# Kernel optimization log

Measured on AMD Instinct MI355X. Metric: run time of the kernel, lower is better.

Reference implementation:

```python
import jax, jax.numpy as jnp
import numpy as np

B, N, D = 32768, 256, 3


def setup_inputs() -> dict:
    key = jax.random.key(0)
    k1, k2 = jax.random.split(key)
    keypoints = jax.random.normal(k1, (B, N, D), dtype=jnp.float32)
    perm = jax.random.permutation(k2, B)  # emulates torch.randperm, deterministic
    return {"keypoints": keypoints, "perm": perm}


def _transform_a2b(src, dst):
    # src, dst: [B, N, 3]; batched similarity (Umeyama/Kabsch-style) alignment.
    num = src.shape[1]
    src_mean = src.mean(axis=1)                     # [B, 3]
    dst_mean = dst.mean(axis=1)                     # [B, 3]
    src_d = src - src_mean[:, None]                 # [B, N, 3]
    dst_d = dst - dst_mean[:, None]                 # [B, N, 3]
    A = jnp.einsum('bni,bnj->bij', dst_d, src_d) / num  # [B, 3, 3] covariance
    U, S, Vt = jnp.linalg.svd(A)
    # NOTE: in the original torch code `d[neg_A][:, -1, -1] = -1` writes into a
    # COPY (advanced indexing), so d stays identity for all batches. We
    # faithfully reproduce that actual behavior: R = U @ V^T, scale uses sum(S).
    var_sum = jnp.mean(jnp.sum(src_d * src_d, axis=-1), axis=1)  # sum of per-dim biased var
    scale = jnp.sum(S, axis=-1) / var_sum           # [B]
    R = U @ Vt                                      # [B, 3, 3]
    T = dst_mean - scale[:, None] * jnp.einsum('bij,bj->bi', R, src_mean)  # [B, 3]
    # Original computes R, scale, T under torch.no_grad().
    R = jax.lax.stop_gradient(R)
    scale = jax.lax.stop_gradient(scale)
    T = jax.lax.stop_gradient(T)
    return src @ (jnp.swapaxes(R, -1, -2) * scale[:, None, None]) + T[:, None]


def reference(keypoints, perm):
    dst = keypoints[perm]                            # randomized keypoints
    trans = _transform_a2b(keypoints, dst)
    return jnp.mean(jnp.abs(trans - dst))
```

## Files before the change

kernel.cpp:

```cpp
#include <hip/hip_runtime.h>
#include <math.h>

#define GEO_N 256

__device__ __forceinline__ float frcp(float x) { return __builtin_amdgcn_rcpf(x); }
__device__ __forceinline__ float frsq(float x) { return __builtin_amdgcn_rsqf(x); }
__device__ __forceinline__ float fsqrtf_(float x) { return __builtin_amdgcn_sqrtf(x); }

__device__ __forceinline__ float wredf(float v) {
#pragma unroll
  for (int off = 32; off; off >>= 1) v += __shfl_xor(v, off, 64);
  return v;
}

template <int P, int Q>
__device__ __forceinline__ void jrot(float G[3][3], float V[3][3]) {
  const float apq = G[P][Q];
  const float tau = (G[Q][Q] - G[P][P]) * 0.5f * frcp(apq);
  const float tt = fsqrtf_(1.0f + tau * tau);
  const float tr = frcp(tau + copysignf(tt, tau));
  const float cr = frsq(1.0f + tr * tr);
  const bool skip = fabsf(apq) < 1e-30f;
  const float c = skip ? 1.0f : cr;
  const float s = skip ? 0.0f : tr * cr;
#pragma unroll
  for (int k = 0; k < 3; ++k) {
    float gkp = G[k][P], gkq = G[k][Q];
    G[k][P] = c * gkp - s * gkq;
    G[k][Q] = s * gkp + c * gkq;
  }
#pragma unroll
  for (int k = 0; k < 3; ++k) {
    float gpk = G[P][k], gqk = G[Q][k];
    G[P][k] = c * gpk - s * gqk;
    G[Q][k] = s * gpk + c * gqk;
  }
#pragma unroll
  for (int k = 0; k < 3; ++k) {
    float vkp = V[k][P], vkq = V[k][Q];
    V[k][P] = c * vkp - s * vkq;
    V[k][Q] = s * vkp + c * vkq;
  }
}

__device__ __forceinline__ void solve_rst(const float s0[16], float bc[13]) {
  const float invN = 1.0f / (float)GEO_N;
  const float smx = s0[0] * invN, smy = s0[1] * invN, smz = s0[2] * invN;
  const float dmx = s0[3] * invN, dmy = s0[4] * invN, dmz = s0[5] * invN;
  float A[3][3];
  A[0][0] = s0[6] * invN - dmx * smx;  A[0][1] = s0[7] * invN - dmx * smy;  A[0][2] = s0[8] * invN - dmx * smz;
  A[1][0] = s0[9] * invN - dmy * smx;  A[1][1] = s0[10] * invN - dmy * smy; A[1][2] = s0[11] * invN - dmy * smz;
  A[2][0] = s0[12] * invN - dmz * smx; A[2][1] = s0[13] * invN - dmz * smy; A[2][2] = s0[14] * invN - dmz * smz;
  const float var_sum = s0[15] * invN - (smx * smx + smy * smy + smz * smz);

  float G[3][3];
#pragma unroll
  for (int i = 0; i < 3; ++i)
#pragma unroll
    for (int j = 0; j < 3; ++j)
      G[i][j] = A[0][i] * A[0][j] + A[1][i] * A[1][j] + A[2][i] * A[2][j];
  float V[3][3] = {{1, 0, 0}, {0, 1, 0}, {0, 0, 1}};
#pragma unroll
  for (int sweep = 0; sweep < 4; ++sweep) {
    jrot<0, 1>(G, V);
    jrot<0, 2>(G, V);
    jrot<1, 2>(G, V);
  }
  float l0 = G[0][0], l1 = G[1][1], l2 = G[2][2];
  if (l0 < l1) { float tl = l0; l0 = l1; l1 = tl;
#pragma unroll
    for (int k = 0; k < 3; ++k) { float tv = V[k][0]; V[k][0] = V[k][1]; V[k][1] = tv; } }
  if (l0 < l2) { float tl = l0; l0 = l2; l2 = tl;
#pragma unroll
    for (int k = 0; k < 3; ++k) { float tv = V[k][0]; V[k][0] = V[k][2]; V[k][2] = tv; } }
  if (l1 < l2) { float tl = l1; l1 = l2; l2 = tl;
#pragma unroll
    for (int k = 0; k < 3; ++k) { float tv = V[k][1]; V[k][1] = V[k][2]; V[k][2] = tv; } }
  const float sig0 = fsqrtf_(fmaxf(l0, 0.0f));
  const float sig1 = fsqrtf_(fmaxf(l1, 0.0f));
  const float sig2 = fsqrtf_(fmaxf(l2, 0.0f));

  float v0[3] = {V[0][0], V[1][0], V[2][0]};
  float v1[3] = {V[0][1], V[1][1], V[2][1]};
  float v2[3] = {V[0][2], V[1][2], V[2][2]};
  float u0[3], u1[3], u2r[3];
#pragma unroll
  for (int i = 0; i < 3; ++i) {
    u0[i]  = A[i][0] * v0[0] + A[i][1] * v0[1] + A[i][2] * v0[2];
    u1[i]  = A[i][0] * v1[0] + A[i][1] * v1[1] + A[i][2] * v1[2];
    u2r[i] = A[i][0] * v2[0] + A[i][1] * v2[1] + A[i][2] * v2[2];
  }
  float n0 = u0[0] * u0[0] + u0[1] * u0[1] + u0[2] * u0[2];
  if (n0 > 1e-28f) { float inv = frsq(n0); u0[0] *= inv; u0[1] *= inv; u0[2] *= inv; }
  else { u0[0] = 1.0f; u0[1] = 0.0f; u0[2] = 0.0f; }
  float d01 = u1[0] * u0[0] + u1[1] * u0[1] + u1[2] * u0[2];
  u1[0] -= d01 * u0[0]; u1[1] -= d01 * u0[1]; u1[2] -= d01 * u0[2];
  float n1 = u1[0] * u1[0] + u1[1] * u1[1] + u1[2] * u1[2];
  if (n1 > 1e-28f) { float inv = frsq(n1); u1[0] *= inv; u1[1] *= inv; u1[2] *= inv; }
  else {
    float ex[3] = {1, 0, 0}, ey[3] = {0, 1, 0};
    const float* e = (fabsf(u0[0]) < 0.9f) ? ex : ey;
    u1[0] = u0[1] * e[2] - u0[2] * e[1];
    u1[1] = u0[2] * e[0] - u0[0] * e[2];
    u1[2] = u0[0] * e[1] - u0[1] * e[0];
    float nn = u1[0] * u1[0] + u1[1] * u1[1] + u1[2] * u1[2];
    float inv = frsq(nn);
    u1[0] *= inv; u1[1] *= inv; u1[2] *= inv;
  }
  float u2[3] = {u0[1] * u1[2] - u0[2] * u1[1],
                 u0[2] * u1[0] - u0[0] * u1[2],
                 u0[0] * u1[1] - u0[1] * u1[0]};
  float d2 = u2[0] * u2r[0] + u2[1] * u2r[1] + u2[2] * u2r[2];
  if (d2 < 0.0f) { u2[0] = -u2[0]; u2[1] = -u2[1]; u2[2] = -u2[2]; }

  const float scale = (sig0 + sig1 + sig2) * frcp(fmaxf(var_sum, 1e-30f));
  float R[3][3];
#pragma unroll
  for (int i = 0; i < 3; ++i)
#pragma unroll
    for (int j = 0; j < 3; ++j)
      R[i][j] = u0[i] * v0[j] + u1[i] * v1[j] + u2[i] * v2[j];
  const float Tx = dmx - scale * (R[0][0] * smx + R[0][1] * smy + R[0][2] * smz);
  const float Ty = dmy - scale * (R[1][0] * smx + R[1][1] * smy + R[1][2] * smz);
  const float Tz = dmz - scale * (R[2][0] * smx + R[2][1] * smy + R[2][2] * smz);
#pragma unroll
  for (int i = 0; i < 3; ++i)
#pragma unroll
    for (int j = 0; j < 3; ++j) bc[3 * i + j] = R[i][j];
  bc[9] = scale; bc[10] = Tx; bc[11] = Ty; bc[12] = Tz;
}

__global__ __launch_bounds__(256) void geo_wave4p(const float* __restrict__ kp,
                                                  const int* __restrict__ perm,
                                                  float* __restrict__ partials,
                                                  int B, int NW) {
  const int wid = (blockIdx.x << 2) | (threadIdx.x >> 6);
  if (wid >= NW) return;
  const int lane = threadIdx.x & 63;
  const int b0 = wid * 4;
  const float4* base = (const float4*)kp;

  int pm[4];
#pragma unroll
  for (int i = 0; i < 4; ++i) pm[i] = perm[min(b0 + i, B - 1)];

  float4 S[4][3], D[4][3];
  float parked = 0.0f;

#define GEO_LOAD(i)                                                        \
  {                                                                        \
    const int bb = min(b0 + (i), B - 1);                                   \
    const float4* s4 = base + (size_t)bb * 192 + lane * 3;                 \
    const float4* d4 = base + (size_t)pm[(i)] * 192 + lane * 3;            \
    S[(i)][0] = s4[0]; S[(i)][1] = s4[1]; S[(i)][2] = s4[2];               \
    D[(i)][0] = d4[0]; D[(i)][1] = d4[1]; D[(i)][2] = d4[2];               \
  }

#define GEO_MOM(i)                                                         \
  {                                                                        \
    const float s_[12] = {S[(i)][0].x, S[(i)][0].y, S[(i)][0].z, S[(i)][0].w, \
                          S[(i)][1].x, S[(i)][1].y, S[(i)][1].z, S[(i)][1].w, \
                          S[(i)][2].x, S[(i)][2].y, S[(i)][2].z, S[(i)][2].w}; \
    const float d_[12] = {D[(i)][0].x, D[(i)][0].y, D[(i)][0].z, D[(i)][0].w, \
                          D[(i)][1].x, D[(i)][1].y, D[(i)][1].z, D[(i)][1].w, \
                          D[(i)][2].x, D[(i)][2].y, D[(i)][2].z, D[(i)][2].w}; \
    float r[16];                                                           \
    _Pragma("unroll") for (int k = 0; k < 16; ++k) r[k] = 0.0f;            \
    _Pragma("unroll") for (int p = 0; p < 4; ++p) {                        \
      const float sx = s_[3 * p + 0], sy = s_[3 * p + 1], sz = s_[3 * p + 2]; \
      const float dx = d_[3 * p + 0], dy = d_[3 * p + 1], dz = d_[3 * p + 2]; \
      r[0] += sx; r[1] += sy; r[2] += sz;                                  \
      r[3] += dx; r[4] += dy; r[5] += dz;                                  \
      r[6] += dx * sx; r[7] += dx * sy; r[8] += dx * sz;                   \
      r[9] += dy * sx; r[10] += dy * sy; r[11] += dy * sz;                 \
      r[12] += dz * sx; r[13] += dz * sy; r[14] += dz * sz;                \
      r[15] += sx * sx + sy * sy + sz * sz;                                \
    }                                                                      \
     \
    const int b1 = lane & 1, b2 = (lane >> 1) & 1, b3 = (lane >> 2) & 1, b4 = (lane >> 3) & 1; \
    float v8[8], v4_[4], v2[2], v1;                                        \
    _Pragma("unroll") for (int k = 0; k < 8; ++k) {                        \
      float send = b1 ? r[k] : r[k + 8];                                   \
      float recv = __shfl_xor(send, 1, 64);                                \
      v8[k] = (b1 ? r[k + 8] : r[k]) + recv;                               \
    }                                                                      \
    _Pragma("unroll") for (int k = 0; k < 4; ++k) {                        \
      float send = b2 ? v8[k] : v8[k + 4];                                 \
      float recv = __shfl_xor(send, 2, 64);                                \
      v4_[k] = (b2 ? v8[k + 4] : v8[k]) + recv;                            \
    }                                                                      \
    _Pragma("unroll") for (int k = 0; k < 2; ++k) {                        \
      float send = b3 ? v4_[k] : v4_[k + 2];                               \
      float recv = __shfl_xor(send, 4, 64);                                \
      v2[k] = (b3 ? v4_[k + 2] : v4_[k]) + recv;                           \
    }                                                                      \
    {                                                                      \
      float send = b4 ? v2[0] : v2[1];                                     \
      float recv = __shfl_xor(send, 8, 64);                                \
      v1 = (b4 ? v2[1] : v2[0]) + recv;                                    \
    }                                                                      \
    v1 += __shfl_xor(v1, 16, 64);                                          \
    v1 += __shfl_xor(v1, 32, 64);                                          \
    if ((lane >> 4) == (i)) parked = v1;                                   \
  }

  GEO_LOAD(0)
  GEO_LOAD(1)
  __builtin_amdgcn_sched_barrier(0);
  GEO_MOM(0)
  GEO_LOAD(2)
  __builtin_amdgcn_sched_barrier(0);
  GEO_MOM(1)
  GEO_LOAD(3)
  __builtin_amdgcn_sched_barrier(0);
  GEO_MOM(2)
  __builtin_amdgcn_sched_barrier(0);
  GEO_MOM(3)

#undef GEO_LOAD
#undef GEO_MOM

  constexpr int br[16] = {0, 8, 4, 12, 2, 10, 6, 14, 1, 9, 5, 13, 3, 11, 7, 15};
  float s0[16];
#pragma unroll
  for (int k = 0; k < 16; ++k)
    s0[k] = __shfl(parked, ((lane & 3) << 4) | br[k], 64);

  float bc[13];
  solve_rst(s0, bc);

  float acc = 0.0f;
#pragma unroll
  for (int i = 0; i < 4; ++i) {
    const float R00 = __shfl(bc[0], i, 64), R01 = __shfl(bc[1], i, 64), R02 = __shfl(bc[2], i, 64);
    const float R10 = __shfl(bc[3], i, 64), R11 = __shfl(bc[4], i, 64), R12 = __shfl(bc[5], i, 64);
    const float R20 = __shfl(bc[6], i, 64), R21 = __shfl(bc[7], i, 64), R22 = __shfl(bc[8], i, 64);
    const float sc  = __shfl(bc[9], i, 64);
    const float Tx  = __shfl(bc[10], i, 64), Ty = __shfl(bc[11], i, 64), Tz = __shfl(bc[12], i, 64);
    const float s[12] = {S[i][0].x, S[i][0].y, S[i][0].z, S[i][0].w,
                         S[i][1].x, S[i][1].y, S[i][1].z, S[i][1].w,
                         S[i][2].x, S[i][2].y, S[i][2].z, S[i][2].w};
    const float d[12] = {D[i][0].x, D[i][0].y, D[i][0].z, D[i][0].w,
                         D[i][1].x, D[i][1].y, D[i][1].z, D[i][1].w,
                         D[i][2].x, D[i][2].y, D[i][2].z, D[i][2].w};
    float a = 0.0f;
#pragma unroll
    for (int q = 0; q < 4; ++q) {
      const float sx = s[3 * q + 0], sy = s[3 * q + 1], sz = s[3 * q + 2];
      const float dx = d[3 * q + 0], dy = d[3 * q + 1], dz = d[3 * q + 2];
      const float e0 = sc * (R00 * sx + R01 * sy + R02 * sz) + Tx - dx;
      const float e1 = sc * (R10 * sx + R11 * sy + R12 * sz) + Ty - dy;
      const float e2 = sc * (R20 * sx + R21 * sy + R22 * sz) + Tz - dz;
      a += fabsf(e0) + fabsf(e1) + fabsf(e2);
    }
    if (b0 + i < B) acc += a;
  }
  acc = wredf(acc);
  if (lane == 0) partials[wid] = acc;
}

__global__ __launch_bounds__(1024) void geo_fin(const float* __restrict__ partials,
                                                float* __restrict__ out, int n,
                                                double inv_total) {
  const int t = threadIdx.x;
  double acc = 0.0;
  for (int i = t; i < n; i += 1024) acc += (double)partials[i];
#pragma unroll
  for (int off = 32; off; off >>= 1) acc += __shfl_xor(acc, off, 64);
  __shared__ double sred[16];
  if ((t & 63) == 0) sred[t >> 6] = acc;
  __syncthreads();
  if (t == 0) {
    double tot = 0.0;
#pragma unroll
    for (int k = 0; k < 16; ++k) tot += sred[k];
    out[0] = (float)(tot * inv_total);
  }
}

extern "C" void kernel_launch(void* const* d_in, const int* in_sizes, int n_in,
                              void* d_out, int out_size, void* d_ws, size_t ws_size,
                              hipStream_t stream) {
  const float* kp = (const float*)d_in[0];
  const int* perm = (const int*)d_in[1];
  float* out = (float*)d_out;
  const int B = in_sizes[1];
  const double inv_total = 1.0 / ((double)B * (double)GEO_N * 3.0);

  const int NW = (B + 3) / 4;
  float* partials = (float*)d_ws;
  const int grid = (NW + 3) / 4;
  geo_wave4p<<<grid, 256, 0, stream>>>(kp, perm, partials, B, NW);
  geo_fin<<<1, 1024, 0, stream>>>(partials, out, NW, inv_total);
}
```

Baseline: 43.44 us.

## Replace Jacobi SVD with closed-form eigen solve and polar rotation

Replaces the 4-sweep Jacobi eigen-decomposition of A^T A with the analytic trigonometric eigenvalue formula for symmetric 3x3 matrices. It uses polynomial approximations of acos and cos, gets two eigenvectors from cross products, and forms R = A (A^T A)^{-1/2} directly instead of building U. This removes many serial rcp/sqrt-heavy rotations per batch in the solve phase. In exchange it risks accuracy for near-degenerate or rank-deficient covariances, and the sign handling differs from the explicit U construction. The v2 rename only avoids a name clash in the macro.

```diff
diff --git a/kernel.cpp b/kernel.cpp
--- a/kernel.cpp
+++ b/kernel.cpp
@@ -13,121 +13,104 @@
   return v;
 }
 
-template <int P, int Q>
-__device__ __forceinline__ void jrot(float G[3][3], float V[3][3]) {
-  const float apq = G[P][Q];
-  const float tau = (G[Q][Q] - G[P][P]) * 0.5f * frcp(apq);
-  const float tt = fsqrtf_(1.0f + tau * tau);
-  const float tr = frcp(tau + copysignf(tt, tau));
-  const float cr = frsq(1.0f + tr * tr);
-  const bool skip = fabsf(apq) < 1e-30f;
-  const float c = skip ? 1.0f : cr;
-  const float s = skip ? 0.0f : tr * cr;
-#pragma unroll
-  for (int k = 0; k < 3; ++k) {
-    float gkp = G[k][P], gkq = G[k][Q];
-    G[k][P] = c * gkp - s * gkq;
-    G[k][Q] = s * gkp + c * gkq;
-  }
-#pragma unroll
-  for (int k = 0; k < 3; ++k) {
-    float gpk = G[P][k], gqk = G[Q][k];
-    G[P][k] = c * gpk - s * gqk;
-    G[Q][k] = s * gpk + c * gqk;
-  }
-#pragma unroll
-  for (int k = 0; k < 3; ++k) {
-    float vkp = V[k][P], vkq = V[k][Q];
-    V[k][P] = c * vkp - s * vkq;
-    V[k][Q] = s * vkp + c * vkq;
-  }
-}
-
-__device__ __forceinline__ void solve_rst(const float s0[16], float bc[13]) {
+__device__ __forceinline__ void eigvec3(float g00, float g01, float g02,
+                                        float g11, float g12, float g22,
+                                        float l, float v[3]) {
+  const float m00 = g00 - l, m11 = g11 - l, m22 = g22 - l;
+  const float a0 = g01 * g12 - g02 * m11, a1 = g02 * g01 - m00 * g12, a2 = m00 * m11 - g01 * g01;
+  const float b0 = g01 * m22 - g02 * g12, b1 = g02 * g02 - m00 * m22, b2 = m00 * g12 - g01 * g02;
+  const float c0 = m11 * m22 - g12 * g12, c1 = g12 * g02 - g01 * m22, c2 = g01 * g12 - m11 * g02;
+  const float na = a0 * a0 + a1 * a1 + a2 * a2;
+  const float nb = b0 * b0 + b1 * b1 + b2 * b2;
+  const float nc = c0 * c0 + c1 * c1 + c2 * c2;
+  float s0 = a0, s1 = a1, s2 = a2, ns = na;
+  if (nb > ns) { s0 = b0; s1 = b1; s2 = b2; ns = nb; }
+  if (nc > ns) { s0 = c0; s1 = c1; s2 = c2; ns = nc; }
+  const bool bad = ns < 1e-28f;
+  const float inv = frsq(fmaxf(ns, 1e-28f));
+  v[0] = bad ? 1.0f : s0 * inv;
+  v[1] = bad ? 0.0f : s1 * inv;
+  v[2] = bad ? 0.0f : s2 * inv;
+}
+
+__device__ __forceinline__ void solve_rst(const float s0in[16], float bc[13]) {
   const float invN = 1.0f / (float)GEO_N;
-  const float smx = s0[0] * invN, smy = s0[1] * invN, smz = s0[2] * invN;
-  const float dmx = s0[3] * invN, dmy = s0[4] * invN, dmz = s0[5] * invN;
-  float A[3][3];
-  A[0][0] = s0[6] * invN - dmx * smx;  A[0][1] = s0[7] * invN - dmx * smy;  A[0][2] = s0[8] * invN - dmx * smz;
-  A[1][0] = s0[9] * invN - dmy * smx;  A[1][1] = s0[10] * invN - dmy * smy; A[1][2] = s0[11] * invN - dmy * smz;
-  A[2][0] = s0[12] * invN - dmz * smx; A[2][1] = s0[13] * invN - dmz * smy; A[2][2] = s0[14] * invN - dmz * smz;
-  const float var_sum = s0[15] * invN - (smx * smx + smy * smy + smz * smz);
-
-  float G[3][3];
-#pragma unroll
-  for (int i = 0; i < 3; ++i)
-#pragma unroll
-    for (int j = 0; j < 3; ++j)
-      G[i][j] = A[0][i] * A[0][j] + A[1][i] * A[1][j] + A[2][i] * A[2][j];
-  float V[3][3] = {{1, 0, 0}, {0, 1, 0}, {0, 0, 1}};
-#pragma unroll
-  for (int sweep = 0; sweep < 4; ++sweep) {
-    jrot<0, 1>(G, V);
-    jrot<0, 2>(G, V);
-    jrot<1, 2>(G, V);
-  }
-  float l0 = G[0][0], l1 = G[1][1], l2 = G[2][2];
-  if (l0 < l1) { float tl = l0; l0 = l1; l1 = tl;
-#pragma unroll
-    for (int k = 0; k < 3; ++k) { float tv = V[k][0]; V[k][0] = V[k][1]; V[k][1] = tv; } }
-  if (l0 < l2) { float tl = l0; l0 = l2; l2 = tl;
-#pragma unroll
-    for (int k = 0; k < 3; ++k) { float tv = V[k][0]; V[k][0] = V[k][2]; V[k][2] = tv; } }
-  if (l1 < l2) { float tl = l1; l1 = l2; l2 = tl;
-#pragma unroll
-    for (int k = 0; k < 3; ++k) { float tv = V[k][1]; V[k][1] = V[k][2]; V[k][2] = tv; } }
-  const float sig0 = fsqrtf_(fmaxf(l0, 0.0f));
-  const float sig1 = fsqrtf_(fmaxf(l1, 0.0f));
-  const float sig2 = fsqrtf_(fmaxf(l2, 0.0f));
-
-  float v0[3] = {V[0][0], V[1][0], V[2][0]};
-  float v1[3] = {V[0][1], V[1][1], V[2][1]};
-  float v2[3] = {V[0][2], V[1][2], V[2][2]};
-  float u0[3], u1[3], u2r[3];
-#pragma unroll
-  for (int i = 0; i < 3; ++i) {
-    u0[i]  = A[i][0] * v0[0] + A[i][1] * v0[1] + A[i][2] * v0[2];
-    u1[i]  = A[i][0] * v1[0] + A[i][1] * v1[1] + A[i][2] * v1[2];
-    u2r[i] = A[i][0] * v2[0] + A[i][1] * v2[1] + A[i][2] * v2[2];
-  }
-  float n0 = u0[0] * u0[0] + u0[1] * u0[1] + u0[2] * u0[2];
-  if (n0 > 1e-28f) { float inv = frsq(n0); u0[0] *= inv; u0[1] *= inv; u0[2] *= inv; }
-  else { u0[0] = 1.0f; u0[1] = 0.0f; u0[2] = 0.0f; }
-  float d01 = u1[0] * u0[0] + u1[1] * u0[1] + u1[2] * u0[2];
-  u1[0] -= d01 * u0[0]; u1[1] -= d01 * u0[1]; u1[2] -= d01 * u0[2];
-  float n1 = u1[0] * u1[0] + u1[1] * u1[1] + u1[2] * u1[2];
-  if (n1 > 1e-28f) { float inv = frsq(n1); u1[0] *= inv; u1[1] *= inv; u1[2] *= inv; }
-  else {
-    float ex[3] = {1, 0, 0}, ey[3] = {0, 1, 0};
-    const float* e = (fabsf(u0[0]) < 0.9f) ? ex : ey;
-    u1[0] = u0[1] * e[2] - u0[2] * e[1];
-    u1[1] = u0[2] * e[0] - u0[0] * e[2];
-    u1[2] = u0[0] * e[1] - u0[1] * e[0];
-    float nn = u1[0] * u1[0] + u1[1] * u1[1] + u1[2] * u1[2];
-    float inv = frsq(nn);
-    u1[0] *= inv; u1[1] *= inv; u1[2] *= inv;
-  }
-  float u2[3] = {u0[1] * u1[2] - u0[2] * u1[1],
-                 u0[2] * u1[0] - u0[0] * u1[2],
-                 u0[0] * u1[1] - u0[1] * u1[0]};
-  float d2 = u2[0] * u2r[0] + u2[1] * u2r[1] + u2[2] * u2r[2];
-  if (d2 < 0.0f) { u2[0] = -u2[0]; u2[1] = -u2[1]; u2[2] = -u2[2]; }
-
-  const float scale = (sig0 + sig1 + sig2) * frcp(fmaxf(var_sum, 1e-30f));
-  float R[3][3];
-#pragma unroll
-  for (int i = 0; i < 3; ++i)
-#pragma unroll
-    for (int j = 0; j < 3; ++j)
-      R[i][j] = u0[i] * v0[j] + u1[i] * v1[j] + u2[i] * v2[j];
-  const float Tx = dmx - scale * (R[0][0] * smx + R[0][1] * smy + R[0][2] * smz);
-  const float Ty = dmy - scale * (R[1][0] * smx + R[1][1] * smy + R[1][2] * smz);
-  const float Tz = dmz - scale * (R[2][0] * smx + R[2][1] * smy + R[2][2] * smz);
-#pragma unroll
-  for (int i = 0; i < 3; ++i)
-#pragma unroll
-    for (int j = 0; j < 3; ++j) bc[3 * i + j] = R[i][j];
-  bc[9] = scale; bc[10] = Tx; bc[11] = Ty; bc[12] = Tz;
+  const float smx = s0in[0] * invN, smy = s0in[1] * invN, smz = s0in[2] * invN;
+  const float dmx = s0in[3] * invN, dmy = s0in[4] * invN, dmz = s0in[5] * invN;
+  const float A00 = s0in[6] * invN - dmx * smx,  A01 = s0in[7] * invN - dmx * smy,  A02 = s0in[8] * invN - dmx * smz;
+  const float A10 = s0in[9] * invN - dmy * smx,  A11 = s0in[10] * invN - dmy * smy, A12 = s0in[11] * invN - dmy * smz;
+  const float A20 = s0in[12] * invN - dmz * smx, A21 = s0in[13] * invN - dmz * smy, A22 = s0in[14] * invN - dmz * smz;
+  const float var_sum = s0in[15] * invN - (smx * smx + smy * smy + smz * smz);
+
+  const float g00 = A00 * A00 + A10 * A10 + A20 * A20;
+  const float g11 = A01 * A01 + A11 * A11 + A21 * A21;
+  const float g22 = A02 * A02 + A12 * A12 + A22 * A22;
+  const float g01 = A00 * A01 + A10 * A11 + A20 * A21;
+  const float g02 = A00 * A02 + A10 * A12 + A20 * A22;
+  const float g12 = A01 * A02 + A11 * A12 + A21 * A22;
+
+  const float q = (g00 + g11 + g22) * (1.0f / 3.0f);
+  const float c00 = g00 - q, c11 = g11 - q, c22 = g22 - q;
+  const float p1 = g01 * g01 + g02 * g02 + g12 * g12;
+  const float p2 = c00 * c00 + c11 * c11 + c22 * c22 + 2.0f * p1;
+  const float p = fsqrtf_(p2 * (1.0f / 6.0f));
+  const float pinv = frcp(fmaxf(p, 1e-20f));
+  const float detC = c00 * (c11 * c22 - g12 * g12)
+                   - g01 * (g01 * c22 - g12 * g02)
+                   + g02 * (g01 * g12 - c11 * g02);
+  float rr = 0.5f * detC * pinv * pinv * pinv;
+  rr = fminf(1.0f, fmaxf(-1.0f, rr));
+  const float arr = fabsf(rr);
+  const float acs = fsqrtf_(fmaxf(1.0f - arr, 0.0f)) *
+      (1.5707288f + arr * (-0.2121144f + arr * (0.0742610f + arr * (-0.0187293f))));
+  const float acr = (rr >= 0.0f) ? acs : (3.14159265f - acs);
+  const float phi = acr * (1.0f / 3.0f);
+  const float x1 = phi * phi;
+  const float cph = 1.0f + x1 * (-0.5f + x1 * ((1.0f / 24.0f) - x1 * (1.0f / 720.0f)));
+  const float uu = 1.04719755f - phi;
+  const float x2 = uu * uu;
+  const float cp3 = -(1.0f + x2 * (-0.5f + x2 * ((1.0f / 24.0f) - x2 * (1.0f / 720.0f))));
+  const float l0 = q + 2.0f * p * cph;
+  const float l2 = q + 2.0f * p * cp3;
+  const float l1 = 3.0f * q - l0 - l2;
+
+  float v0[3], v2[3];
+  eigvec3(g00, g01, g02, g11, g12, g22, l0, v0);
+  eigvec3(g00, g01, g02, g11, g12, g22, l2, v2);
+
+  const float sg0 = fsqrtf_(fmaxf(l0, 0.0f));
+  const float sg1 = fsqrtf_(fmaxf(l1, 0.0f));
+  const float sg2 = fsqrtf_(fmaxf(l2, 0.0f));
+  const float iv0 = (sg0 > 1e-20f) ? frcp(sg0) : 0.0f;
+  const float iv1 = (sg1 > 1e-20f) ? frcp(sg1) : 0.0f;
+  const float iv2 = (sg2 > 1e-20f) ? frcp(sg2) : 0.0f;
+
+  const float da = iv0 - iv1, db = iv2 - iv1;
+  const float w00 = iv1 + da * v0[0] * v0[0] + db * v2[0] * v2[0];
+  const float w11 = iv1 + da * v0[1] * v0[1] + db * v2[1] * v2[1];
+  const float w22 = iv1 + da * v0[2] * v0[2] + db * v2[2] * v2[2];
+  const float w01 = da * v0[0] * v0[1] + db * v2[0] * v2[1];
+  const float w02 = da * v0[0] * v0[2] + db * v2[0] * v2[2];
+  const float w12 = da * v0[1] * v0[2] + db * v2[1] * v2[2];
+
+  const float R00 = A00 * w00 + A01 * w01 + A02 * w02;
+  const float R01 = A00 * w01 + A01 * w11 + A02 * w12;
+  const float R02 = A00 * w02 + A01 * w12 + A02 * w22;
+  const float R10 = A10 * w00 + A11 * w01 + A12 * w02;
+  const float R11 = A10 * w01 + A11 * w11 + A12 * w12;
+  const float R12 = A10 * w02 + A11 * w12 + A12 * w22;
+  const float R20 = A20 * w00 + A21 * w01 + A22 * w02;
+  const float R21 = A20 * w01 + A21 * w11 + A22 * w12;
+  const float R22 = A20 * w02 + A21 * w12 + A22 * w22;
+
+  const float scale = (sg0 + sg1 + sg2) * frcp(fmaxf(var_sum, 1e-30f));
+  bc[0] = R00; bc[1] = R01; bc[2] = R02;
+  bc[3] = R10; bc[4] = R11; bc[5] = R12;
+  bc[6] = R20; bc[7] = R21; bc[8] = R22;
+  bc[9] = scale;
+  bc[10] = dmx - scale * (R00 * smx + R01 * smy + R02 * smz);
+  bc[11] = dmy - scale * (R10 * smx + R11 * smy + R12 * smz);
+  bc[12] = dmz - scale * (R20 * smx + R21 * smy + R22 * smz);
 }
 
 __global__ __launch_bounds__(256) void geo_wave4p(const float* __restrict__ kp,
@@ -176,9 +159,8 @@
       r[12] += dz * sx; r[13] += dz * sy; r[14] += dz * sz;                \
       r[15] += sx * sx + sy * sy + sz * sz;                                \
     }                                                                      \
-     \
     const int b1 = lane & 1, b2 = (lane >> 1) & 1, b3 = (lane >> 2) & 1, b4 = (lane >> 3) & 1; \
-    float v8[8], v4_[4], v2[2], v1;                                        \
+    float v8[8], v4_[4], v2_[2], v1;                                       \
     _Pragma("unroll") for (int k = 0; k < 8; ++k) {                        \
       float send = b1 ? r[k] : r[k + 8];                                   \
       float recv = __shfl_xor(send, 1, 64);                                \
@@ -192,12 +174,12 @@
     _Pragma("unroll") for (int k = 0; k < 2; ++k) {                        \
       float send = b3 ? v4_[k] : v4_[k + 2];                               \
       float recv = __shfl_xor(send, 4, 64);                                \
-      v2[k] = (b3 ? v4_[k + 2] : v4_[k]) + recv;                           \
+      v2_[k] = (b3 ? v4_[k + 2] : v4_[k]) + recv;                          \
     }                                                                      \
     {                                                                      \
-      float send = b4 ? v2[0] : v2[1];                                     \
+      float send = b4 ? v2_[0] : v2_[1];                                   \
       float recv = __shfl_xor(send, 8, 64);                                \
-      v1 = (b4 ? v2[1] : v2[0]) + recv;                                    \
+      v1 = (b4 ? v2_[1] : v2_[0]) + recv;                                  \
     }                                                                      \
     v1 += __shfl_xor(v1, 16, 64);                                          \
     v1 += __shfl_xor(v1, 32, 64);                                          \
```

New measurement: 39.77 us. 1.09x faster.
